# Performance work log

Measured on AMD Instinct MI355X. Metric: run time of the kernel, lower is better.

## Reference

```python
import jax, jax.numpy as jnp
import numpy as np

IN_FEATURES = 8192
OUT_FEATURES = 8192
BATCH = 256


def setup_inputs() -> dict:
    key = jax.random.key(0)
    k_x, k_w, k_s, k_b = jax.random.split(key, 4)
    x = jax.random.normal(k_x, (BATCH, IN_FEATURES), dtype=jnp.float32)
    int8_weights = jax.random.randint(k_w, (OUT_FEATURES, IN_FEATURES), -128, 128, dtype=jnp.int8)
    int8_scales = jax.random.normal(k_s, (1,), dtype=jnp.float32)
    bias = jax.random.normal(k_b, (1, OUT_FEATURES), dtype=jnp.float32)
    return {"x": x, "int8_weights": int8_weights, "int8_scales": int8_scales, "bias": bias}


def reference(x, int8_weights, int8_scales, bias):
    # dequantize: symmetric per-tensor scale, then cast to activation dtype
    weights = int8_weights.astype(x.dtype) * int8_scales.astype(x.dtype)  # [out, in]
    # F.linear: x @ W^T
    out = jnp.einsum('bi,oi->bo', x, weights)
    out = out + bias
    return out
```

## Files before the change

### kernel.cpp

```cpp
#include <hip/hip_runtime.h>

#define M_DIM 256
#define N_DIM 8192
#define K_DIM 8192
#define BN 128
#define BK 32
#define KSPLIT 4
#define KLEN (K_DIM / KSPLIT)
#define NT (KLEN / BK)
#define ABYTES 16384
#define BBYTES 8192
#define BUFB (ABYTES + BBYTES)

typedef _Float16 half_t;
typedef __attribute__((ext_vector_type(8))) _Float16 half8;
typedef __attribute__((ext_vector_type(4))) float f32x4;
typedef __attribute__((ext_vector_type(4))) unsigned int u32x4;

__device__ __forceinline__ unsigned int pk2(float a, float b) {
  return __builtin_bit_cast(unsigned int, __builtin_amdgcn_cvt_pkrtz(a, b));
}
__device__ __forceinline__ void gl16(const void* g, void* l) {
  __builtin_amdgcn_global_load_lds(
      (const __attribute__((address_space(1))) unsigned int*)g,
      (__attribute__((address_space(3))) unsigned int*)l, 16, 0, 0);
}

__global__ __launch_bounds__(256) void convert_x(const float* __restrict__ x,
                                                 half_t* __restrict__ xh) {
  const int gid = blockIdx.x * 256 + threadIdx.x;
  const int row = gid >> 10;
  const int k0 = (gid & 1023) << 3;
  float4 v0 = *(const float4*)(x + (size_t)row * K_DIM + k0);
  float4 v1 = *(const float4*)(x + (size_t)row * K_DIM + k0 + 4);
  half8 h;
  h[0] = (half_t)v0.x; h[1] = (half_t)v0.y; h[2] = (half_t)v0.z; h[3] = (half_t)v0.w;
  h[4] = (half_t)v1.x; h[5] = (half_t)v1.y; h[6] = (half_t)v1.z; h[7] = (half_t)v1.w;
  const int kt = k0 >> 5, kk = k0 & 31;
  *(half8*)(xh + (size_t)kt * 8192 + row * 32 + kk) = h;
}

__global__ __launch_bounds__(512, 2) void qgemm(
    const half_t* __restrict__ xh, const int* __restrict__ Wq,
    const float* __restrict__ scales, const float* __restrict__ bias,
    float* __restrict__ out) {
  __shared__ __align__(1024) char lds[2 * BUFB];

  const int tid = threadIdx.x;
  const int bid = blockIdx.x;
  const int p = bid & 7;
  const int g = bid >> 3;
  const int ks = p >> 1;
  const int t = (g << 1) | (p & 1);
  const int col0 = t * BN;

  const int wid = tid >> 6, lane = tid & 63;
  const int wm = wid >> 1, wn = wid & 1;
  const int r16 = lane & 15, g4 = lane >> 4;

  const half_t* abase = xh + (size_t)(ks * NT) * 8192;
  const int wr = tid >> 2, wc = tid & 3;
  const int* wp0 = Wq + (size_t)(col0 + wr) * K_DIM + ks * KLEN + wc * 8;
  const int wlds = ABYTES + wr * 64 + wc * 16;

  int aoff[4], boff[4];
#pragma unroll
  for (int mf = 0; mf < 4; ++mf) aoff[mf] = (wm * 64 + mf * 16 + r16) * 64 + g4 * 16;
#pragma unroll
  for (int nf = 0; nf < 4; ++nf) boff[nf] = ABYTES + (wn * 64 + nf * 16 + r16) * 64 + g4 * 16;

  f32x4 acc[4][4];
#pragma unroll
  for (int i = 0; i < 4; ++i)
#pragma unroll
    for (int j = 0; j < 4; ++j) acc[i][j] = (f32x4){0.f, 0.f, 0.f, 0.f};

  int4 Wa, Wb;
  {
    int4 w0a = *(const int4*)(wp0);
    int4 w0b = *(const int4*)(wp0 + 4);
    gl16(abase + tid * 8, lds + tid * 16);
    gl16(abase + 4096 + tid * 8, lds + 8192 + tid * 16);
    __builtin_amdgcn_sched_barrier(0);
    u32x4 pb;
    pb.x = pk2((float)w0a.x, (float)w0a.y); pb.y = pk2((float)w0a.z, (float)w0a.w);
    pb.z = pk2((float)w0b.x, (float)w0b.y); pb.w = pk2((float)w0b.z, (float)w0b.w);
    *(u32x4*)(lds + wlds) = pb;
    Wa = *(const int4*)(wp0 + 32);
    Wb = *(const int4*)(wp0 + 36);
    __builtin_amdgcn_sched_barrier(0);
    asm volatile("s_waitcnt vmcnt(2) lgkmcnt(0)" ::: "memory");
    __builtin_amdgcn_s_barrier();
  }

  for (int kt = 0; kt < NT; ++kt) {
    char* Bc = lds + (kt & 1) * BUFB;
    char* Bn = lds + ((kt & 1) ^ 1) * BUFB;

    u32x4 pb;
    pb.x = pk2((float)Wa.x, (float)Wa.y); pb.y = pk2((float)Wa.z, (float)Wa.w);
    pb.z = pk2((float)Wb.x, (float)Wb.y); pb.w = pk2((float)Wb.z, (float)Wb.w);
    *(u32x4*)(Bn + wlds) = pb;

    const int an = (kt + 1 < NT) ? kt + 1 : NT - 1;
    const half_t* asrc = abase + (size_t)an * 8192;
    gl16(asrc + tid * 8, Bn + tid * 16);
    gl16(asrc + 4096 + tid * 8, Bn + 8192 + tid * 16);
    __builtin_amdgcn_sched_barrier(0);

    const int w2 = (kt + 2 < NT) ? kt + 2 : NT - 1;
    Wa = *(const int4*)(wp0 + (size_t)w2 * 32);
    Wb = *(const int4*)(wp0 + (size_t)w2 * 32 + 4);

    half8 af[4], bf[4];
#pragma unroll
    for (int mf = 0; mf < 4; ++mf) af[mf] = *(const half8*)(Bc + aoff[mf]);
#pragma unroll
    for (int nf = 0; nf < 4; ++nf) bf[nf] = *(const half8*)(Bc + boff[nf]);
#pragma unroll
    for (int mf = 0; mf < 4; ++mf)
#pragma unroll
      for (int nf = 0; nf < 4; ++nf)
        acc[mf][nf] = __builtin_amdgcn_mfma_f32_16x16x32_f16(
            af[mf], bf[nf], acc[mf][nf], 0, 0, 0);

    __builtin_amdgcn_sched_barrier(0);
    asm volatile("s_waitcnt vmcnt(2) lgkmcnt(0)" ::: "memory");
    __builtin_amdgcn_s_barrier();
  }

  const float scale = scales[0];
#pragma unroll
  for (int nf = 0; nf < 4; ++nf) {
    const int gcol = col0 + wn * 64 + nf * 16 + r16;
    const float bv = (ks == 0) ? bias[gcol] : 0.0f;
#pragma unroll
    for (int mf = 0; mf < 4; ++mf) {
      const int grow0 = wm * 64 + mf * 16 + g4 * 4;
#pragma unroll
      for (int j = 0; j < 4; ++j) {
        atomicAdd(out + (size_t)(grow0 + j) * N_DIM + gcol,
                  scale * acc[mf][nf][j] + bv);
      }
    }
  }
}

extern "C" void kernel_launch(void* const* d_in, const int* in_sizes, int n_in,
                              void* d_out, int out_size, void* d_ws, size_t ws_size,
                              hipStream_t stream) {
  const float* x = (const float*)d_in[0];
  const int* Wq = (const int*)d_in[1];
  const float* scales = (const float*)d_in[2];
  const float* bias = (const float*)d_in[3];
  float* out = (float*)d_out;
  half_t* xh = (half_t*)d_ws;

  hipMemsetAsync(d_out, 0, (size_t)M_DIM * N_DIM * sizeof(float), stream);
  convert_x<<<dim3(1024), dim3(256), 0, stream>>>(x, xh);
  qgemm<<<dim3(256), dim3(512), 0, stream>>>(xh, Wq, scales, bias, out);
}
```

Baseline: 423.3 us.

## Halve N tile, quad-buffer LDS, swizzle layouts, double grid size

```diff
diff --git a/kernel.cpp b/kernel.cpp
--- a/kernel.cpp
+++ b/kernel.cpp
@@ -3,19 +3,19 @@
 #define M_DIM 256
 #define N_DIM 8192
 #define K_DIM 8192
-#define BN 128
+#define BN 64
 #define BK 32
 #define KSPLIT 4
 #define KLEN (K_DIM / KSPLIT)
 #define NT (KLEN / BK)
-#define ABYTES 16384
-#define BBYTES 8192
-#define BUFB (ABYTES + BBYTES)
+#define ABY 16384
+#define BBY 4096
+#define BUFB (ABY + BBY)
 
 typedef _Float16 half_t;
 typedef __attribute__((ext_vector_type(8))) _Float16 half8;
 typedef __attribute__((ext_vector_type(4))) float f32x4;
-typedef __attribute__((ext_vector_type(4))) unsigned int u32x4;
+typedef __attribute__((ext_vector_type(2))) unsigned int u32x2;
 
 __device__ __forceinline__ unsigned int pk2(float a, float b) {
   return __builtin_bit_cast(unsigned int, __builtin_amdgcn_cvt_pkrtz(a, b));
@@ -36,22 +36,22 @@
   half8 h;
   h[0] = (half_t)v0.x; h[1] = (half_t)v0.y; h[2] = (half_t)v0.z; h[3] = (half_t)v0.w;
   h[4] = (half_t)v1.x; h[5] = (half_t)v1.y; h[6] = (half_t)v1.z; h[7] = (half_t)v1.w;
-  const int kt = k0 >> 5, kk = k0 & 31;
-  *(half8*)(xh + (size_t)kt * 8192 + row * 32 + kk) = h;
+  const int kt = k0 >> 5;
+  const int cx = ((k0 >> 3) & 3) ^ ((row >> 1) & 3);
+  *(half8*)(xh + (size_t)kt * 8192 + row * 32 + cx * 8) = h;
 }
 
-__global__ __launch_bounds__(512, 2) void qgemm(
+__global__ __launch_bounds__(512, 4) void qgemm(
     const half_t* __restrict__ xh, const int* __restrict__ Wq,
     const float* __restrict__ scales, const float* __restrict__ bias,
     float* __restrict__ out) {
-  __shared__ __align__(1024) char lds[2 * BUFB];
+  __shared__ __align__(1024) char lds[4 * BUFB];
 
   const int tid = threadIdx.x;
   const int bid = blockIdx.x;
   const int p = bid & 7;
-  const int g = bid >> 3;
   const int ks = p >> 1;
-  const int t = (g << 1) | (p & 1);
+  const int t = ((bid >> 3) << 1) | (p & 1);
   const int col0 = t * BN;
 
   const int wid = tid >> 6, lane = tid & 63;
@@ -59,80 +59,112 @@
   const int r16 = lane & 15, g4 = lane >> 4;
 
   const half_t* abase = xh + (size_t)(ks * NT) * 8192;
-  const int wr = tid >> 2, wc = tid & 3;
-  const int* wp0 = Wq + (size_t)(col0 + wr) * K_DIM + ks * KLEN + wc * 8;
-  const int wlds = ABYTES + wr * 64 + wc * 16;
+  const int wr = tid >> 3, wc = tid & 7;
+  const int* wp0 = Wq + (size_t)(col0 + wr) * K_DIM + ks * KLEN + wc * 4;
+  const int wlds = ABY + wr * 64 + (((wc >> 1) ^ ((wr >> 1) & 3)) << 4) + ((wc & 1) << 3);
 
-  int aoff[4], boff[4];
+  int aoff[4], boff[2];
 #pragma unroll
-  for (int mf = 0; mf < 4; ++mf) aoff[mf] = (wm * 64 + mf * 16 + r16) * 64 + g4 * 16;
+  for (int mf = 0; mf < 4; ++mf) {
+    int ra = wm * 64 + mf * 16 + r16;
+    aoff[mf] = ra * 64 + ((g4 ^ ((ra >> 1) & 3)) << 4);
+  }
 #pragma unroll
-  for (int nf = 0; nf < 4; ++nf) boff[nf] = ABYTES + (wn * 64 + nf * 16 + r16) * 64 + g4 * 16;
+  for (int nf = 0; nf < 2; ++nf) {
+    int rb = wn * 32 + nf * 16 + r16;
+    boff[nf] = ABY + rb * 64 + ((g4 ^ ((rb >> 1) & 3)) << 4);
+  }
 
-  f32x4 acc[4][4];
+  f32x4 acc[4][2];
 #pragma unroll
   for (int i = 0; i < 4; ++i)
 #pragma unroll
-    for (int j = 0; j < 4; ++j) acc[i][j] = (f32x4){0.f, 0.f, 0.f, 0.f};
+    for (int j = 0; j < 2; ++j) acc[i][j] = (f32x4){0.f, 0.f, 0.f, 0.f};
 
-  int4 Wa, Wb;
+  int4 Wset0, Wset1, Wset2, Wset3;
+
+  Wset0 = *(const int4*)(wp0);
+  __builtin_amdgcn_sched_barrier(0);
+  gl16(abase + tid * 8, lds + tid * 16);
+  gl16(abase + 4096 + tid * 8, lds + 8192 + tid * 16);
+  __builtin_amdgcn_sched_barrier(0);
+  Wset1 = *(const int4*)(wp0 + 32);
+  __builtin_amdgcn_sched_barrier(0);
+  gl16(abase + 8192 + tid * 8, lds + BUFB + tid * 16);
+  gl16(abase + 8192 + 4096 + tid * 8, lds + BUFB + 8192 + tid * 16);
+  __builtin_amdgcn_sched_barrier(0);
+  Wset2 = *(const int4*)(wp0 + 64);
+  __builtin_amdgcn_sched_barrier(0);
+  asm volatile("s_waitcnt vmcnt(6)" ::: "memory");
   {
-    int4 w0a = *(const int4*)(wp0);
-    int4 w0b = *(const int4*)(wp0 + 4);
-    gl16(abase + tid * 8, lds + tid * 16);
-    gl16(abase + 4096 + tid * 8, lds + 8192 + tid * 16);
-    __builtin_amdgcn_sched_barrier(0);
-    u32x4 pb;
-    pb.x = pk2((float)w0a.x, (float)w0a.y); pb.y = pk2((float)w0a.z, (float)w0a.w);
-    pb.z = pk2((float)w0b.x, (float)w0b.y); pb.w = pk2((float)w0b.z, (float)w0b.w);
-    *(u32x4*)(lds + wlds) = pb;
-    Wa = *(const int4*)(wp0 + 32);
-    Wb = *(const int4*)(wp0 + 36);
-    __builtin_amdgcn_sched_barrier(0);
-    asm volatile("s_waitcnt vmcnt(2) lgkmcnt(0)" ::: "memory");
-    __builtin_amdgcn_s_barrier();
+    u32x2 pb;
+    pb.x = pk2((float)Wset0.x, (float)Wset0.y);
+    pb.y = pk2((float)Wset0.z, (float)Wset0.w);
+    *(u32x2*)(lds + wlds) = pb;
+  }
+  __builtin_amdgcn_sched_barrier(0);
+  asm volatile("s_waitcnt vmcnt(4) lgkmcnt(0)" ::: "memory");
+  __builtin_amdgcn_s_barrier();
+  __builtin_amdgcn_sched_barrier(0);
+
+#define ONE_ITER(KT, C0, C1, C2, C3)                                          \
+  {                                                                           \
+    asm volatile("s_waitcnt vmcnt(3)" ::: "memory");                          \
+    __builtin_amdgcn_sched_barrier(0);                                        \
+    {                                                                         \
+      u32x2 pb;                                                               \
+      pb.x = pk2((float)Wset##C1.x, (float)Wset##C1.y);                       \
+      pb.y = pk2((float)Wset##C1.z, (float)Wset##C1.w);                       \
+      *(u32x2*)(lds + (C1)*BUFB + wlds) = pb;                                 \
+    }                                                                         \
+    __builtin_amdgcn_sched_barrier(0);                                        \
+    {                                                                         \
+      const int an = ((KT) + 2 < NT) ? (KT) + 2 : NT - 1;                     \
+      const half_t* asrc = abase + (size_t)an * 8192;                         \
+      gl16(asrc + tid * 8, lds + (C2)*BUFB + tid * 16);                       \
+      gl16(asrc + 4096 + tid * 8, lds + (C2)*BUFB + 8192 + tid * 16);         \
+    }                                                                         \
+    __builtin_amdgcn_sched_barrier(0);                                        \
+    {                                                                         \
+      const int w3 = ((KT) + 3 < NT) ? (KT) + 3 : NT - 1;                     \
+      Wset##C3 = *(const int4*)(wp0 + (size_t)w3 * 32);                       \
+    }                                                                         \
+    __builtin_amdgcn_sched_barrier(0);                                        \
+    {                                                                         \
+      const char* Bc = lds + (C0)*BUFB;                                       \
+      half8 af0 = *(const half8*)(Bc + aoff[0]);                              \
+      half8 af1 = *(const half8*)(Bc + aoff[1]);                              \
+      half8 af2 = *(const half8*)(Bc + aoff[2]);                              \
+      half8 af3 = *(const half8*)(Bc + aoff[3]);                              \
+      half8 bf0 = *(const half8*)(Bc + boff[0]);                              \
+      half8 bf1 = *(const half8*)(Bc + boff[1]);                              \
+      acc[0][0] = __builtin_amdgcn_mfma_f32_16x16x32_f16(af0, bf0, acc[0][0], 0, 0, 0); \
+      acc[0][1] = __builtin_amdgcn_mfma_f32_16x16x32_f16(af0, bf1, acc[0][1], 0, 0, 0); \
+      acc[1][0] = __builtin_amdgcn_mfma_f32_16x16x32_f16(af1, bf0, acc[1][0], 0, 0, 0); \
+      acc[1][1] = __builtin_amdgcn_mfma_f32_16x16x32_f16(af1, bf1, acc[1][1], 0, 0, 0); \
+      acc[2][0] = __builtin_amdgcn_mfma_f32_16x16x32_f16(af2, bf0, acc[2][0], 0, 0, 0); \
+      acc[2][1] = __builtin_amdgcn_mfma_f32_16x16x32_f16(af2, bf1, acc[2][1], 0, 0, 0); \
+      acc[3][0] = __builtin_amdgcn_mfma_f32_16x16x32_f16(af3, bf0, acc[3][0], 0, 0, 0); \
+      acc[3][1] = __builtin_amdgcn_mfma_f32_16x16x32_f16(af3, bf1, acc[3][1], 0, 0, 0); \
+    }                                                                         \
+    __builtin_amdgcn_sched_barrier(0);                                        \
+    asm volatile("s_waitcnt vmcnt(4) lgkmcnt(0)" ::: "memory");               \
+    __builtin_amdgcn_s_barrier();                                             \
+    __builtin_amdgcn_sched_barrier(0);                                        \
   }
 
-  for (int kt = 0; kt < NT; ++kt) {
-    char* Bc = lds + (kt & 1) * BUFB;
-    char* Bn = lds + ((kt & 1) ^ 1) * BUFB;
-
-    u32x4 pb;
-    pb.x = pk2((float)Wa.x, (float)Wa.y); pb.y = pk2((float)Wa.z, (float)Wa.w);
-    pb.z = pk2((float)Wb.x, (float)Wb.y); pb.w = pk2((float)Wb.z, (float)Wb.w);
-    *(u32x4*)(Bn + wlds) = pb;
-
-    const int an = (kt + 1 < NT) ? kt + 1 : NT - 1;
-    const half_t* asrc = abase + (size_t)an * 8192;
-    gl16(asrc + tid * 8, Bn + tid * 16);
-    gl16(asrc + 4096 + tid * 8, Bn + 8192 + tid * 16);
-    __builtin_amdgcn_sched_barrier(0);
-
-    const int w2 = (kt + 2 < NT) ? kt + 2 : NT - 1;
-    Wa = *(const int4*)(wp0 + (size_t)w2 * 32);
-    Wb = *(const int4*)(wp0 + (size_t)w2 * 32 + 4);
-
-    half8 af[4], bf[4];
-#pragma unroll
-    for (int mf = 0; mf < 4; ++mf) af[mf] = *(const half8*)(Bc + aoff[mf]);
-#pragma unroll
-    for (int nf = 0; nf < 4; ++nf) bf[nf] = *(const half8*)(Bc + boff[nf]);
-#pragma unroll
-    for (int mf = 0; mf < 4; ++mf)
-#pragma unroll
-      for (int nf = 0; nf < 4; ++nf)
-        acc[mf][nf] = __builtin_amdgcn_mfma_f32_16x16x32_f16(
-            af[mf], bf[nf], acc[mf][nf], 0, 0, 0);
-
-    __builtin_amdgcn_sched_barrier(0);
-    asm volatile("s_waitcnt vmcnt(2) lgkmcnt(0)" ::: "memory");
-    __builtin_amdgcn_s_barrier();
+  for (int kt0 = 0; kt0 < NT; kt0 += 4) {
+    ONE_ITER(kt0 + 0, 0, 1, 2, 3)
+    ONE_ITER(kt0 + 1, 1, 2, 3, 0)
+    ONE_ITER(kt0 + 2, 2, 3, 0, 1)
+    ONE_ITER(kt0 + 3, 3, 0, 1, 2)
   }
+#undef ONE_ITER
 
   const float scale = scales[0];
 #pragma unroll
-  for (int nf = 0; nf < 4; ++nf) {
-    const int gcol = col0 + wn * 64 + nf * 16 + r16;
+  for (int nf = 0; nf < 2; ++nf) {
+    const int gcol = col0 + wn * 32 + nf * 16 + r16;
     const float bv = (ks == 0) ? bias[gcol] : 0.0f;
 #pragma unroll
     for (int mf = 0; mf < 4; ++mf) {
@@ -158,5 +190,5 @@
 
   hipMemsetAsync(d_out, 0, (size_t)M_DIM * N_DIM * sizeof(float), stream);
   convert_x<<<dim3(1024), dim3(256), 0, stream>>>(x, xh);
-  qgemm<<<dim3(256), dim3(512), 0, stream>>>(xh, Wq, scales, bias, out);
+  qgemm<<<dim3(512), dim3(512), 0, stream>>>(xh, Wq, scales, bias, out);
 }
```

Result: faster. 408.6 us (-3.5%).

## Stream int8 weights straight to registers and stage full-batch X chunks in swizzled LDS

Applied to the files above, without the earlier changes.

```diff
diff --git a/kernel.cpp b/kernel.cpp
--- a/kernel.cpp
+++ b/kernel.cpp
@@ -3,14 +3,11 @@
 #define M_DIM 256
 #define N_DIM 8192
 #define K_DIM 8192
-#define BN 128
-#define BK 32
 #define KSPLIT 4
 #define KLEN (K_DIM / KSPLIT)
-#define NT (KLEN / BK)
-#define ABYTES 16384
-#define BBYTES 8192
-#define BUFB (ABYTES + BBYTES)
+#define NC (KLEN / 128)
+#define CHE 32768
+#define CHB 65536
 
 typedef _Float16 half_t;
 typedef __attribute__((ext_vector_type(8))) _Float16 half8;
@@ -36,113 +33,116 @@
   half8 h;
   h[0] = (half_t)v0.x; h[1] = (half_t)v0.y; h[2] = (half_t)v0.z; h[3] = (half_t)v0.w;
   h[4] = (half_t)v1.x; h[5] = (half_t)v1.y; h[6] = (half_t)v1.z; h[7] = (half_t)v1.w;
-  const int kt = k0 >> 5, kk = k0 & 31;
-  *(half8*)(xh + (size_t)kt * 8192 + row * 32 + kk) = h;
+  const int kc = k0 >> 7;
+  const int c16 = (k0 >> 3) & 15;
+  *(half8*)(xh + (size_t)kc * CHE + row * 128 + ((c16 ^ (row & 7)) << 3)) = h;
 }
 
 __global__ __launch_bounds__(512, 2) void qgemm(
     const half_t* __restrict__ xh, const int* __restrict__ Wq,
     const float* __restrict__ scales, const float* __restrict__ bias,
     float* __restrict__ out) {
-  __shared__ __align__(1024) char lds[2 * BUFB];
+  __shared__ __align__(1024) char lds[2 * CHB];
 
   const int tid = threadIdx.x;
   const int bid = blockIdx.x;
   const int p = bid & 7;
-  const int g = bid >> 3;
   const int ks = p >> 1;
-  const int t = (g << 1) | (p & 1);
-  const int col0 = t * BN;
+  const int t = ((bid >> 3) << 1) | (p & 1);
+  const int col0 = t * 128;
 
   const int wid = tid >> 6, lane = tid & 63;
-  const int wm = wid >> 1, wn = wid & 1;
   const int r16 = lane & 15, g4 = lane >> 4;
+  const int n0 = col0 + wid * 16;
 
-  const half_t* abase = xh + (size_t)(ks * NT) * 8192;
-  const int wr = tid >> 2, wc = tid & 3;
-  const int* wp0 = Wq + (size_t)(col0 + wr) * K_DIM + ks * KLEN + wc * 8;
-  const int wlds = ABYTES + wr * 64 + wc * 16;
+  const int* wp = Wq + (size_t)(n0 + r16) * K_DIM + ks * KLEN + g4 * 8;
+  const half_t* xbase = xh + (size_t)(ks * NC) * CHE;
 
-  int aoff[4], boff[4];
+  int rb[4];
 #pragma unroll
-  for (int mf = 0; mf < 4; ++mf) aoff[mf] = (wm * 64 + mf * 16 + r16) * 64 + g4 * 16;
+  for (int ks4 = 0; ks4 < 4; ++ks4)
+    rb[ks4] = r16 * 256 + ((((ks4 << 2) + g4) ^ (r16 & 7)) << 4);
+
+  f32x4 acc[16];
 #pragma unroll
-  for (int nf = 0; nf < 4; ++nf) boff[nf] = ABYTES + (wn * 64 + nf * 16 + r16) * 64 + g4 * 16;
+  for (int i = 0; i < 16; ++i) acc[i] = (f32x4){0.f, 0.f, 0.f, 0.f};
 
-  f32x4 acc[4][4];
+  int4 sA[8], sB[8];
+
 #pragma unroll
-  for (int i = 0; i < 4; ++i)
+  for (int i = 0; i < 8; ++i)
+    gl16(xbase + (tid + i * 512) * 8, lds + (tid + i * 512) * 16);
+  __builtin_amdgcn_sched_barrier(0);
 #pragma unroll
-    for (int j = 0; j < 4; ++j) acc[i][j] = (f32x4){0.f, 0.f, 0.f, 0.f};
+  for (int ks4 = 0; ks4 < 4; ++ks4) {
+    sA[2 * ks4] = *(const int4*)(wp + ks4 * 32);
+    sA[2 * ks4 + 1] = *(const int4*)(wp + ks4 * 32 + 4);
+  }
+#pragma unroll
+  for (int ks4 = 0; ks4 < 4; ++ks4) {
+    sB[2 * ks4] = *(const int4*)(wp + 128 + ks4 * 32);
+    sB[2 * ks4 + 1] = *(const int4*)(wp + 128 + ks4 * 32 + 4);
+  }
+  __builtin_amdgcn_sched_barrier(0);
+  asm volatile("s_waitcnt vmcnt(8)" ::: "memory");
+  __builtin_amdgcn_s_barrier();
 
-  int4 Wa, Wb;
-  {
-    int4 w0a = *(const int4*)(wp0);
-    int4 w0b = *(const int4*)(wp0 + 4);
-    gl16(abase + tid * 8, lds + tid * 16);
-    gl16(abase + 4096 + tid * 8, lds + 8192 + tid * 16);
-    __builtin_amdgcn_sched_barrier(0);
-    u32x4 pb;
-    pb.x = pk2((float)w0a.x, (float)w0a.y); pb.y = pk2((float)w0a.z, (float)w0a.w);
-    pb.z = pk2((float)w0b.x, (float)w0b.y); pb.w = pk2((float)w0b.z, (float)w0b.w);
-    *(u32x4*)(lds + wlds) = pb;
-    Wa = *(const int4*)(wp0 + 32);
-    Wb = *(const int4*)(wp0 + 36);
-    __builtin_amdgcn_sched_barrier(0);
-    asm volatile("s_waitcnt vmcnt(2) lgkmcnt(0)" ::: "memory");
+#define CHUNK(C, SET, STAGE, PREF)                                            \
+  {                                                                           \
+    const char* bufc = lds + ((C) & 1) * CHB;                                 \
+    if (STAGE) {                                                              \
+      char* bn = lds + (((C) + 1) & 1) * CHB;                                 \
+      const half_t* src = xbase + (size_t)((C) + 1) * CHE;                    \
+      _Pragma("unroll") for (int i = 0; i < 8; ++i)                           \
+          gl16(src + (tid + i * 512) * 8, bn + (tid + i * 512) * 16);         \
+    }                                                                         \
+    __builtin_amdgcn_sched_barrier(0);                                        \
+    _Pragma("unroll") for (int ks4 = 0; ks4 < 4; ++ks4) {                     \
+      int4 w0 = SET[2 * ks4], w1 = SET[2 * ks4 + 1];                          \
+      if (PREF) {    \
+        const int* q = wp + ((C) + 2) * 128 + ks4 * 32;                       \
+        SET[2 * ks4] = *(const int4*)q;                                       \
+        SET[2 * ks4 + 1] = *(const int4*)(q + 4);                             \
+      }                                                                       \
+      u32x4 au;                                                               \
+      au.x = pk2((float)w0.x, (float)w0.y);                                   \
+      au.y = pk2((float)w0.z, (float)w0.w);                                   \
+      au.z = pk2((float)w1.x, (float)w1.y);                                   \
+      au.w = pk2((float)w1.z, (float)w1.w);                                   \
+      half8 af = __builtin_bit_cast(half8, au);                               \
+      _Pragma("unroll") for (int mt = 0; mt < 16; ++mt) {                     \
+        half8 bf = *(const half8*)(bufc + mt * 4096 + rb[ks4]);               \
+        acc[mt] = __builtin_amdgcn_mfma_f32_16x16x32_f16(af, bf, acc[mt], 0, 0, 0); \
+      }                                                                       \
+    }                                                                         \
+    __builtin_amdgcn_sched_barrier(0);                                        \
+  }
+
+  for (int pr = 0; pr < 7; ++pr) {
+    CHUNK(2 * pr, sA, 1, 1)
+    asm volatile("s_waitcnt vmcnt(8)" ::: "memory");
+    __builtin_amdgcn_s_barrier();
+    CHUNK(2 * pr + 1, sB, 1, 1)
+    asm volatile("s_waitcnt vmcnt(8)" ::: "memory");
     __builtin_amdgcn_s_barrier();
   }
-
-  for (int kt = 0; kt < NT; ++kt) {
-    char* Bc = lds + (kt & 1) * BUFB;
-    char* Bn = lds + ((kt & 1) ^ 1) * BUFB;
-
-    u32x4 pb;
-    pb.x = pk2((float)Wa.x, (float)Wa.y); pb.y = pk2((float)Wa.z, (float)Wa.w);
-    pb.z = pk2((float)Wb.x, (float)Wb.y); pb.w = pk2((float)Wb.z, (float)Wb.w);
-    *(u32x4*)(Bn + wlds) = pb;
-
-    const int an = (kt + 1 < NT) ? kt + 1 : NT - 1;
-    const half_t* asrc = abase + (size_t)an * 8192;
-    gl16(asrc + tid * 8, Bn + tid * 16);
-    gl16(asrc + 4096 + tid * 8, Bn + 8192 + tid * 16);
-    __builtin_amdgcn_sched_barrier(0);
-
-    const int w2 = (kt + 2 < NT) ? kt + 2 : NT - 1;
-    Wa = *(const int4*)(wp0 + (size_t)w2 * 32);
-    Wb = *(const int4*)(wp0 + (size_t)w2 * 32 + 4);
-
-    half8 af[4], bf[4];
-#pragma unroll
-    for (int mf = 0; mf < 4; ++mf) af[mf] = *(const half8*)(Bc + aoff[mf]);
-#pragma unroll
-    for (int nf = 0; nf < 4; ++nf) bf[nf] = *(const half8*)(Bc + boff[nf]);
-#pragma unroll
-    for (int mf = 0; mf < 4; ++mf)
-#pragma unroll
-      for (int nf = 0; nf < 4; ++nf)
-        acc[mf][nf] = __builtin_amdgcn_mfma_f32_16x16x32_f16(
-            af[mf], bf[nf], acc[mf][nf], 0, 0, 0);
-
-    __builtin_amdgcn_sched_barrier(0);
-    asm volatile("s_waitcnt vmcnt(2) lgkmcnt(0)" ::: "memory");
-    __builtin_amdgcn_s_barrier();
-  }
+  CHUNK(14, sA, 1, 0)
+  asm volatile("s_waitcnt vmcnt(0)" ::: "memory");
+  __builtin_amdgcn_s_barrier();
+  CHUNK(15, sB, 0, 0)
+#undef CHUNK
 
   const float scale = scales[0];
+  float4 bv4 = {0.f, 0.f, 0.f, 0.f};
+  if (ks == 0) bv4 = *(const float4*)(bias + n0 + g4 * 4);
 #pragma unroll
-  for (int nf = 0; nf < 4; ++nf) {
-    const int gcol = col0 + wn * 64 + nf * 16 + r16;
-    const float bv = (ks == 0) ? bias[gcol] : 0.0f;
-#pragma unroll
-    for (int mf = 0; mf < 4; ++mf) {
-      const int grow0 = wm * 64 + mf * 16 + g4 * 4;
-#pragma unroll
-      for (int j = 0; j < 4; ++j) {
-        atomicAdd(out + (size_t)(grow0 + j) * N_DIM + gcol,
-                  scale * acc[mf][nf][j] + bv);
-      }
-    }
+  for (int mt = 0; mt < 16; ++mt) {
+    const int m = mt * 16 + r16;
+    float* orow = out + (size_t)m * N_DIM + n0 + g4 * 4;
+    atomicAdd(orow + 0, scale * acc[mt][0] + bv4.x);
+    atomicAdd(orow + 1, scale * acc[mt][1] + bv4.y);
+    atomicAdd(orow + 2, scale * acc[mt][2] + bv4.z);
+    atomicAdd(orow + 3, scale * acc[mt][3] + bv4.w);
   }
 }
 
```

Result: slower. 500.4 us (+18.2%).
